# Kernel optimization log

Hardware: AMD Instinct MI355X
Metric: run time of the kernel (lower is better)

The kernel has to match this reference:

```python
import jax, jax.numpy as jnp
import numpy as np

ALPHA = 0.25
GAMMA = 2.0
EPS = 1e-8
W_CLASS = 2.0
W_BBOX = 5.0
W_GIOU = 2.0
PROB_THRESH = 0.5
BBOX_THRESH = -0.1
BIG = 1e9  # cost assigned to filtered-out (masked) pseudo targets


def box_cxcywh_to_xyxy(b):
    cx, cy, w, h = b[..., 0], b[..., 1], b[..., 2], b[..., 3]
    return jnp.stack([cx - 0.5 * w, cy - 0.5 * h, cx + 0.5 * w, cy + 0.5 * h], axis=-1)


def generalized_box_iou(boxes1, boxes2):
    # boxes1: [..., N, 4] xyxy, boxes2: [..., M, 4] xyxy -> [..., N, M]
    area1 = (boxes1[..., 2] - boxes1[..., 0]) * (boxes1[..., 3] - boxes1[..., 1])
    area2 = (boxes2[..., 2] - boxes2[..., 0]) * (boxes2[..., 3] - boxes2[..., 1])
    lt = jnp.maximum(boxes1[..., :, None, :2], boxes2[..., None, :, :2])
    rb = jnp.minimum(boxes1[..., :, None, 2:], boxes2[..., None, :, 2:])
    wh = jnp.clip(rb - lt, 0.0)
    inter = wh[..., 0] * wh[..., 1]
    union = area1[..., :, None] + area2[..., None, :] - inter
    iou = inter / union
    lt_c = jnp.minimum(boxes1[..., :, None, :2], boxes2[..., None, :, :2])
    rb_c = jnp.maximum(boxes1[..., :, None, 2:], boxes2[..., None, :, 2:])
    wh_c = jnp.clip(rb_c - lt_c, 0.0)
    area_c = wh_c[..., 0] * wh_c[..., 1]
    return iou - (area_c - union) / area_c


def setup_inputs() -> dict:
    key = jax.random.key(0)
    k1, k2, k3, k4, k5 = jax.random.split(key, 5)
    B, Q, C, T = 32, 900, 91, 30
    return {
        "pred_logits": jax.random.normal(k1, (B, Q, C), dtype=jnp.float32),
        "pred_boxes": jax.random.uniform(k2, (B, Q, 4), dtype=jnp.float32),
        "pred_logits_base": jax.random.normal(k3, (B, Q, C), dtype=jnp.float32),
        "pred_boxes_base": jax.random.uniform(k4, (B, Q, 4), dtype=jnp.float32),
        "targets_boxes": jax.random.uniform(k5, (B, T, 4), dtype=jnp.float32),
    }


def reference(pred_logits, pred_boxes, pred_logits_base, pred_boxes_base, targets_boxes):
    # ---- pseudo-label generation from the base model (original: sort + python filter) ----
    prob_base = jax.nn.sigmoid(pred_logits_base)          # [B, Qb, C]
    top_prob = jnp.max(prob_base, axis=-1)                # [B, Qb]
    pseudo_labels = jnp.argmax(prob_base, axis=-1)        # [B, Qb] (idx_base[..., 0])
    keep_prob = top_prob > PROB_THRESH
    # original per-box loop: keep if all(-giou(pseudo, gt) > bbox_thresh)
    g_pt = generalized_box_iou(box_cxcywh_to_xyxy(pred_boxes_base),
                               box_cxcywh_to_xyxy(targets_boxes))  # [B, Qb, T]
    keep_giou = jnp.all(-g_pt > BBOX_THRESH, axis=-1)     # [B, Qb]
    pseudo_mask = keep_prob & keep_giou                   # valid pseudo-target slots

    # ---- cost matrix between current predictions and pseudo targets ----
    out_prob = jax.nn.sigmoid(pred_logits)                # [B, Q, C]
    # gather class prob at each pseudo target's label: [B, Q, Qb]
    p = jnp.take_along_axis(out_prob, pseudo_labels[:, None, :], axis=2)
    pos_cost = ALPHA * (1.0 - p) ** GAMMA * (-jnp.log(p + EPS))
    neg_cost = (1.0 - ALPHA) * p ** GAMMA * (-jnp.log(1.0 - p + EPS))
    cost_class = pos_cost - neg_cost

    # L1 cdist between cxcywh boxes: [B, Q, Qb]
    cost_bbox = jnp.sum(jnp.abs(pred_boxes[:, :, None, :] - pred_boxes_base[:, None, :, :]), axis=-1)

    cost_giou = -generalized_box_iou(box_cxcywh_to_xyxy(pred_boxes),
                                     box_cxcywh_to_xyxy(pred_boxes_base))  # [B, Q, Qb]

    C = W_BBOX * cost_bbox + W_CLASS * cost_class + W_GIOU * cost_giou
    # masked (filtered-out) pseudo targets get a huge cost so they are never matched
    C = jnp.where(pseudo_mask[:, None, :], C, BIG)
    return C, pseudo_mask
```

## Files before the change

### kernel.cpp

```cpp
#include <hip/hip_runtime.h>

static constexpr int B  = 32;
static constexpr int Q  = 900;
static constexpr int NC = 91;
static constexpr int T  = 30;
static constexpr int QT = 12;

static constexpr float ALPHA_  = 0.25f;
static constexpr float EPS_    = 1e-8f;
static constexpr float BIG_    = 1e9f;

__global__ __launch_bounds__(256) void k1_mask_label(
    const float* __restrict__ logits_base,
    const float4* __restrict__ boxes_base,
    const float4* __restrict__ targets,
    int* __restrict__ labels,
    float* __restrict__ mask_out) {
#pragma clang fp contract(off)
  int wid  = (blockIdx.x * blockDim.x + threadIdx.x) >> 6;
  int lane = threadIdx.x & 63;
  if (wid >= B * Q) return;
  int b = wid / Q;

  const float* row = logits_base + (size_t)wid * NC;
  float v  = (lane < NC) ? row[lane] : -1e30f;
  int  arg = lane;
  int lane2 = lane + 64;
  if (lane2 < NC) {
    float v2 = row[lane2];
    if (v2 > v) { v = v2; arg = lane2; }
  }
  for (int off = 32; off >= 1; off >>= 1) {
    float ov = __shfl_xor(v, off, 64);
    int   oi = __shfl_xor(arg, off, 64);
    if (ov > v || (ov == v && oi < arg)) { v = ov; arg = oi; }
  }
  bool keep = (v > 0.0f);

  float4 bb = boxes_base[wid];
  float x1 = bb.x - 0.5f * bb.z, y1 = bb.y - 0.5f * bb.w;
  float x2 = bb.x + 0.5f * bb.z, y2 = bb.y + 0.5f * bb.w;
  float a1 = (x2 - x1) * (y2 - y1);

  bool ok = true;
  if (lane < T) {
    float4 tb = targets[b * T + lane];
    float tx1 = tb.x - 0.5f * tb.z, ty1 = tb.y - 0.5f * tb.w;
    float tx2 = tb.x + 0.5f * tb.z, ty2 = tb.y + 0.5f * tb.w;
    float a2 = (tx2 - tx1) * (ty2 - ty1);
    float ltx = fmaxf(x1, tx1), lty = fmaxf(y1, ty1);
    float rbx = fminf(x2, tx2), rby = fminf(y2, ty2);
    float iw = fmaxf(rbx - ltx, 0.0f), ih = fmaxf(rby - lty, 0.0f);
    float inter = iw * ih;
    float uni = (a1 + a2) - inter;
    float iou = inter / uni;
    float cx1 = fminf(x1, tx1), cy1 = fminf(y1, ty1);
    float cx2 = fmaxf(x2, tx2), cy2 = fmaxf(y2, ty2);
    float cw = fmaxf(cx2 - cx1, 0.0f), ch = fmaxf(cy2 - cy1, 0.0f);
    float ac = cw * ch;
    float g = iou - (ac - uni) / ac;
    ok = (-g > -0.1f);
  }
  keep = keep && __all(ok);

  if (lane == 0) {
    labels[wid]   = arg;
    mask_out[wid] = keep ? 1.0f : 0.0f;
  }
}

__device__ __forceinline__ float class_cost(float x) {
  float p   = __builtin_amdgcn_rcpf(1.0f + __expf(-x));
  float omp = 1.0f - p;
  float pos = ALPHA_ * (omp * omp) * (-__logf(p + EPS_));
  float neg = (1.0f - ALPHA_) * (p * p) * (-__logf(omp + EPS_));
  return pos - neg;
}

__global__ __launch_bounds__(256) void k2_class_cost(
    const float4* __restrict__ lg, float4* __restrict__ cc, int n4) {
  int i = blockIdx.x * 256 + threadIdx.x;
  if (i < n4) {
    float4 v = lg[i];
    float4 o;
    o.x = class_cost(v.x);
    o.y = class_cost(v.y);
    o.z = class_cost(v.z);
    o.w = class_cost(v.w);
    cc[i] = o;
  }
}

__global__ __launch_bounds__(256) void k3_cost(
    const float* __restrict__ cc_all,
    const float4* __restrict__ pred_boxes,
    const float4* __restrict__ boxes_base,
    const int* __restrict__ labels,
    const float* __restrict__ mask_in,
    float* __restrict__ Cout) {
  __shared__ float  s_cc[QT * NC];
  __shared__ float4 s_row[QT][2];
  __shared__ float  s_pa[QT];

  int b   = blockIdx.x / (Q / QT);
  int q0  = (blockIdx.x % (Q / QT)) * QT;
  int tid = threadIdx.x;

  const float4* ccs = reinterpret_cast<const float4*>(
      cc_all + ((size_t)(b * Q + q0)) * NC);
  float4* sc4 = reinterpret_cast<float4*>(s_cc);
  for (int i = tid; i < QT * NC / 4; i += 256) sc4[i] = ccs[i];

  if (tid < QT) {
    float4 pb = pred_boxes[b * Q + q0 + tid];
    float px1 = pb.x - 0.5f * pb.z, py1 = pb.y - 0.5f * pb.w;
    float px2 = pb.x + 0.5f * pb.z, py2 = pb.y + 0.5f * pb.w;
    s_row[tid][0] = pb;
    s_row[tid][1] = make_float4(px1, py1, px2, py2);
    s_pa[tid] = (px2 - px1) * (py2 - py1);
  }

  bool active = (tid < Q / 4);
  float cxb[4], cyb[4], wbx[4], hbx[4], x1b[4], y1b[4], x2b[4], y2b[4], ab[4];
  float c2big[4];
  int lb[4];
  int jbase = b * Q + 4 * tid;
  if (active) {
    int4 lbv = *reinterpret_cast<const int4*>(labels + jbase);
    float4 mkv = *reinterpret_cast<const float4*>(mask_in + jbase);
    lb[0] = lbv.x; lb[1] = lbv.y; lb[2] = lbv.z; lb[3] = lbv.w;
    c2big[0] = 2.0f + (mkv.x != 0.0f ? 0.0f : BIG_);
    c2big[1] = 2.0f + (mkv.y != 0.0f ? 0.0f : BIG_);
    c2big[2] = 2.0f + (mkv.z != 0.0f ? 0.0f : BIG_);
    c2big[3] = 2.0f + (mkv.w != 0.0f ? 0.0f : BIG_);
#pragma unroll
    for (int k = 0; k < 4; ++k) {
      float4 bb = boxes_base[jbase + k];
      cxb[k] = bb.x; cyb[k] = bb.y; wbx[k] = bb.z; hbx[k] = bb.w;
      x1b[k] = bb.x - 0.5f * bb.z; y1b[k] = bb.y - 0.5f * bb.w;
      x2b[k] = bb.x + 0.5f * bb.z; y2b[k] = bb.y + 0.5f * bb.w;
      ab[k]  = (x2b[k] - x1b[k]) * (y2b[k] - y1b[k]);
    }
  }
  __syncthreads();

  if (active) {
    size_t rowbase = ((size_t)(b * Q + q0)) * Q + 4 * tid;
#pragma unroll
    for (int qi = 0; qi < QT; ++qi, rowbase += Q) {
      float4 pc = s_row[qi][0];
      float4 pe = s_row[qi][1];
      float pa  = s_pa[qi];
      const float* ccq = s_cc + qi * NC;
      float res[4];
#pragma unroll
      for (int k = 0; k < 4; ++k) {
        float cls = ccq[lb[k]];
        float l1 = fabsf(pc.x - cxb[k]) + fabsf(pc.y - cyb[k]) +
                   fabsf(pc.z - wbx[k]) + fabsf(pc.w - hbx[k]);
        float mwx = fminf(pe.z, x2b[k]) - fmaxf(pe.x, x1b[k]);
        float mwy = fminf(pe.w, y2b[k]) - fmaxf(pe.y, y1b[k]);
        float iw = fmaxf(mwx, 0.0f), ih = fmaxf(mwy, 0.0f);
        float inter = iw * ih;
        float uni = (pa + ab[k]) - inter;
        float cw = (pc.z + wbx[k]) - mwx;
        float ch = (pc.w + hbx[k]) - mwy;
        float acl = cw * ch;
        float r = __builtin_amdgcn_rcpf(uni * acl);
        float t = (inter * acl + uni * uni) * r;
        res[k] = fmaf(-2.0f, t, fmaf(5.0f, l1, fmaf(2.0f, cls, c2big[k])));
      }
      *reinterpret_cast<float4*>(Cout + rowbase) =
          make_float4(res[0], res[1], res[2], res[3]);
    }
  }
}

extern "C" void kernel_launch(void* const* d_in, const int* in_sizes, int n_in,
                              void* d_out, int out_size, void* d_ws, size_t ws_size,
                              hipStream_t stream) {
  const float*  pred_logits      = (const float*)d_in[0];
  const float4* pred_boxes       = (const float4*)d_in[1];
  const float*  pred_logits_base = (const float*)d_in[2];
  const float4* pred_boxes_base  = (const float4*)d_in[3];
  const float4* targets          = (const float4*)d_in[4];

  float* out      = (float*)d_out;
  float* mask_out = out + (size_t)B * Q * Q;

  int*   labels = (int*)d_ws;
  float* cc     = (float*)((char*)d_ws + 131072);

  k1_mask_label<<<(B * Q * 64) / 256, 256, 0, stream>>>(
      pred_logits_base, pred_boxes_base, targets, labels, mask_out);

  int n4 = B * Q * NC / 4;
  k2_class_cost<<<(n4 + 255) / 256, 256, 0, stream>>>(
      (const float4*)pred_logits, (float4*)cc, n4);

  k3_cost<<<B * (Q / QT), 256, 0, stream>>>(
      cc, pred_boxes, pred_boxes_base, labels, mask_out, out);
}
```

Measured before the change: 49.86 us.

## Merge mask/label and class-cost kernels; nontemporal stores and leaner cost math

Runs the pseudo-label/mask kernel and the class-cost kernel as a single launch with block-range dispatch, removing one launch and letting the two independent workloads overlap. The cost kernel now uses nontemporal loads and stores for the streamed class-cost and output data. It also precomputes per-label shared-memory pointers and simplifies the L1/GIoU arithmetic with FMAs. It sets launch_bounds occupancy to 4. Rounding changes slightly because of the reassociated L1 and union math.

New measurement: 47.43 us. 1.05x faster.

```diff
diff --git a/kernel.cpp b/kernel.cpp
--- a/kernel.cpp
+++ b/kernel.cpp
@@ -1,4 +1,6 @@
 #include <hip/hip_runtime.h>
+
+typedef float f32x4 __attribute__((ext_vector_type(4)));
 
 static constexpr int B  = 32;
 static constexpr int Q  = 900;
@@ -6,20 +8,29 @@
 static constexpr int T  = 30;
 static constexpr int QT = 12;
 
-static constexpr float ALPHA_  = 0.25f;
-static constexpr float EPS_    = 1e-8f;
-static constexpr float BIG_    = 1e9f;
-
-__global__ __launch_bounds__(256) void k1_mask_label(
-    const float* __restrict__ logits_base,
-    const float4* __restrict__ boxes_base,
-    const float4* __restrict__ targets,
-    int* __restrict__ labels,
-    float* __restrict__ mask_out) {
+static constexpr float ALPHA_ = 0.25f;
+static constexpr float EPS_   = 1e-8f;
+static constexpr float BIG_   = 1e9f;
+
+static constexpr int K1_BLOCKS = (B * Q) / 4;
+static constexpr int N4        = B * Q * NC / 4;
+static constexpr int K2_BLOCKS = (N4 + 255) / 256;
+
+__device__ __forceinline__ float class_cost(float x) {
+  float p   = __builtin_amdgcn_rcpf(1.0f + __expf(-x));
+  float omp = 1.0f - p;
+  float pos = ALPHA_ * (omp * omp) * (-__logf(p + EPS_));
+  float neg = (1.0f - ALPHA_) * (p * p) * (-__logf(omp + EPS_));
+  return pos - neg;
+}
+
+__device__ void mask_label_body(int wid, int lane,
+                                const float* __restrict__ logits_base,
+                                const float4* __restrict__ boxes_base,
+                                const float4* __restrict__ targets,
+                                int* __restrict__ labels,
+                                float* __restrict__ mask_out) {
 #pragma clang fp contract(off)
-  int wid  = (blockIdx.x * blockDim.x + threadIdx.x) >> 6;
-  int lane = threadIdx.x & 63;
-  if (wid >= B * Q) return;
   int b = wid / Q;
 
   const float* row = logits_base + (size_t)wid * NC;
@@ -69,29 +80,34 @@
   }
 }
 
-__device__ __forceinline__ float class_cost(float x) {
-  float p   = __builtin_amdgcn_rcpf(1.0f + __expf(-x));
-  float omp = 1.0f - p;
-  float pos = ALPHA_ * (omp * omp) * (-__logf(p + EPS_));
-  float neg = (1.0f - ALPHA_) * (p * p) * (-__logf(omp + EPS_));
-  return pos - neg;
-}
-
-__global__ __launch_bounds__(256) void k2_class_cost(
-    const float4* __restrict__ lg, float4* __restrict__ cc, int n4) {
-  int i = blockIdx.x * 256 + threadIdx.x;
-  if (i < n4) {
-    float4 v = lg[i];
-    float4 o;
-    o.x = class_cost(v.x);
-    o.y = class_cost(v.y);
-    o.z = class_cost(v.z);
-    o.w = class_cost(v.w);
-    cc[i] = o;
-  }
-}
-
-__global__ __launch_bounds__(256) void k3_cost(
+__global__ __launch_bounds__(256) void k12(
+    const float* __restrict__ logits_base,
+    const float4* __restrict__ boxes_base,
+    const float4* __restrict__ targets,
+    int* __restrict__ labels,
+    float* __restrict__ mask_out,
+    const f32x4* __restrict__ lg4,
+    f32x4* __restrict__ cc4) {
+  int tid = threadIdx.x;
+  if (blockIdx.x < K1_BLOCKS) {
+    int wid = (blockIdx.x * 256 + tid) >> 6;
+    mask_label_body(wid, tid & 63, logits_base, boxes_base, targets,
+                    labels, mask_out);
+  } else {
+    int i = (blockIdx.x - K1_BLOCKS) * 256 + tid;
+    if (i < N4) {
+      f32x4 v = __builtin_nontemporal_load(lg4 + i);
+      f32x4 o;
+      o.x = class_cost(v.x);
+      o.y = class_cost(v.y);
+      o.z = class_cost(v.z);
+      o.w = class_cost(v.w);
+      cc4[i] = o;
+    }
+  }
+}
+
+__global__ __launch_bounds__(256, 4) void k3_cost(
     const float* __restrict__ cc_all,
     const float4* __restrict__ pred_boxes,
     const float4* __restrict__ boxes_base,
@@ -99,36 +115,38 @@
     const float* __restrict__ mask_in,
     float* __restrict__ Cout) {
   __shared__ float  s_cc[QT * NC];
-  __shared__ float4 s_row[QT][2];
+  __shared__ float4 s_e[QT];
+  __shared__ float4 s_m[QT];
   __shared__ float  s_pa[QT];
 
   int b   = blockIdx.x / (Q / QT);
   int q0  = (blockIdx.x % (Q / QT)) * QT;
   int tid = threadIdx.x;
 
-  const float4* ccs = reinterpret_cast<const float4*>(
+  const f32x4* ccs = reinterpret_cast<const f32x4*>(
       cc_all + ((size_t)(b * Q + q0)) * NC);
-  float4* sc4 = reinterpret_cast<float4*>(s_cc);
-  for (int i = tid; i < QT * NC / 4; i += 256) sc4[i] = ccs[i];
+  f32x4* sc4 = reinterpret_cast<f32x4*>(s_cc);
+  for (int i = tid; i < QT * NC / 4; i += 256)
+    sc4[i] = __builtin_nontemporal_load(ccs + i);
 
   if (tid < QT) {
     float4 pb = pred_boxes[b * Q + q0 + tid];
     float px1 = pb.x - 0.5f * pb.z, py1 = pb.y - 0.5f * pb.w;
     float px2 = pb.x + 0.5f * pb.z, py2 = pb.y + 0.5f * pb.w;
-    s_row[tid][0] = pb;
-    s_row[tid][1] = make_float4(px1, py1, px2, py2);
+    s_e[tid]  = make_float4(px1, py1, px2, py2);
+    s_m[tid]  = make_float4(px1 + px2, py1 + py2, pb.z, pb.w);
     s_pa[tid] = (px2 - px1) * (py2 - py1);
   }
 
   bool active = (tid < Q / 4);
-  float cxb[4], cyb[4], wbx[4], hbx[4], x1b[4], y1b[4], x2b[4], y2b[4], ab[4];
-  float c2big[4];
-  int lb[4];
+  float x1b[4], y1b[4], x2b[4], y2b[4], wb[4], hb[4], c2big[4];
+  const float* pk[4];
   int jbase = b * Q + 4 * tid;
   if (active) {
     int4 lbv = *reinterpret_cast<const int4*>(labels + jbase);
     float4 mkv = *reinterpret_cast<const float4*>(mask_in + jbase);
-    lb[0] = lbv.x; lb[1] = lbv.y; lb[2] = lbv.z; lb[3] = lbv.w;
+    pk[0] = s_cc + lbv.x; pk[1] = s_cc + lbv.y;
+    pk[2] = s_cc + lbv.z; pk[3] = s_cc + lbv.w;
     c2big[0] = 2.0f + (mkv.x != 0.0f ? 0.0f : BIG_);
     c2big[1] = 2.0f + (mkv.y != 0.0f ? 0.0f : BIG_);
     c2big[2] = 2.0f + (mkv.z != 0.0f ? 0.0f : BIG_);
@@ -136,10 +154,9 @@
 #pragma unroll
     for (int k = 0; k < 4; ++k) {
       float4 bb = boxes_base[jbase + k];
-      cxb[k] = bb.x; cyb[k] = bb.y; wbx[k] = bb.z; hbx[k] = bb.w;
       x1b[k] = bb.x - 0.5f * bb.z; y1b[k] = bb.y - 0.5f * bb.w;
       x2b[k] = bb.x + 0.5f * bb.z; y2b[k] = bb.y + 0.5f * bb.w;
-      ab[k]  = (x2b[k] - x1b[k]) * (y2b[k] - y1b[k]);
+      wb[k]  = bb.z; hb[k] = bb.w;
     }
   }
   __syncthreads();
@@ -148,30 +165,32 @@
     size_t rowbase = ((size_t)(b * Q + q0)) * Q + 4 * tid;
 #pragma unroll
     for (int qi = 0; qi < QT; ++qi, rowbase += Q) {
-      float4 pc = s_row[qi][0];
-      float4 pe = s_row[qi][1];
-      float pa  = s_pa[qi];
-      const float* ccq = s_cc + qi * NC;
+      float4 pe = s_e[qi];
+      float4 pm = s_m[qi];
+      float  pa = s_pa[qi];
       float res[4];
 #pragma unroll
       for (int k = 0; k < 4; ++k) {
-        float cls = ccq[lb[k]];
-        float l1 = fabsf(pc.x - cxb[k]) + fabsf(pc.y - cyb[k]) +
-                   fabsf(pc.z - wbx[k]) + fabsf(pc.w - hbx[k]);
+        float cls = pk[k][qi * NC];
+        float dx = pm.x - (x1b[k] + x2b[k]);
+        float dy = pm.y - (y1b[k] + y2b[k]);
+        float dw = pm.z - wb[k];
+        float dh = pm.w - hb[k];
+        float l1 = fmaf(0.5f, fabsf(dx) + fabsf(dy), fabsf(dw) + fabsf(dh));
         float mwx = fminf(pe.z, x2b[k]) - fmaxf(pe.x, x1b[k]);
         float mwy = fminf(pe.w, y2b[k]) - fmaxf(pe.y, y1b[k]);
-        float iw = fmaxf(mwx, 0.0f), ih = fmaxf(mwy, 0.0f);
-        float inter = iw * ih;
-        float uni = (pa + ab[k]) - inter;
-        float cw = (pc.z + wbx[k]) - mwx;
-        float ch = (pc.w + hbx[k]) - mwy;
+        float inter = fmaxf(mwx, 0.0f) * fmaxf(mwy, 0.0f);
+        float uni = fmaf(wb[k], hb[k], pa) - inter;
+        float cw = (pm.z + wb[k]) - mwx;
+        float ch = (pm.w + hb[k]) - mwy;
         float acl = cw * ch;
         float r = __builtin_amdgcn_rcpf(uni * acl);
-        float t = (inter * acl + uni * uni) * r;
+        float t = fmaf(inter, acl, uni * uni) * r;
         res[k] = fmaf(-2.0f, t, fmaf(5.0f, l1, fmaf(2.0f, cls, c2big[k])));
       }
-      *reinterpret_cast<float4*>(Cout + rowbase) =
-          make_float4(res[0], res[1], res[2], res[3]);
+      f32x4 out4 = {res[0], res[1], res[2], res[3]};
+      __builtin_nontemporal_store(out4,
+          reinterpret_cast<f32x4*>(Cout + rowbase));
     }
   }
 }
@@ -191,12 +210,9 @@
   int*   labels = (int*)d_ws;
   float* cc     = (float*)((char*)d_ws + 131072);
 
-  k1_mask_label<<<(B * Q * 64) / 256, 256, 0, stream>>>(
-      pred_logits_base, pred_boxes_base, targets, labels, mask_out);
-
-  int n4 = B * Q * NC / 4;
-  k2_class_cost<<<(n4 + 255) / 256, 256, 0, stream>>>(
-      (const float4*)pred_logits, (float4*)cc, n4);
+  k12<<<K1_BLOCKS + K2_BLOCKS, 256, 0, stream>>>(
+      pred_logits_base, pred_boxes_base, targets, labels, mask_out,
+      (const f32x4*)pred_logits, (f32x4*)cc);
 
   k3_cost<<<B * (Q / QT), 256, 0, stream>>>(
       cc, pred_boxes, pred_boxes_base, labels, mask_out, out);
```
